# Kernel tuning notes

Hardware: AMD Instinct MI355X
Metric: run time of the kernel (lower is better)

## Reference

```python
import jax, jax.numpy as jnp
import numpy as np

N = 4096      # nodes
F = 32        # num_features (GATConv in = out per head)
H = 2         # heads
NHID = 64     # per-branch mlp output
C = 10        # num_classes
J = 3         # wavelet filters
E = 65536     # edges (avg degree 16)
G = 13        # num_gat = (3**3 - 1) // 2
NEG_SLOPE = 0.2


def setup_inputs() -> dict:
    key = jax.random.key(0)
    ks = jax.random.split(key, 12)
    sc = np.float32(1.0 / np.sqrt(N))
    g = np.float32(0.1)
    x = jax.random.normal(ks[0], (N, F), jnp.float32)
    edge_index = jax.random.randint(ks[1], (2, E), 0, N)
    U = jax.random.normal(ks[2], (N, N), jnp.float32) * sc
    psi = jax.random.normal(ks[3], (J, N, N), jnp.float32) * sc
    # 13 GATConv(F, F, heads=H) parameter stacks
    gat_W = jax.random.normal(ks[4], (G, F, H * F), jnp.float32) * g
    att_src = jax.random.normal(ks[5], (G, H, F), jnp.float32) * g
    att_dst = jax.random.normal(ks[6], (G, H, F), jnp.float32) * g
    gat_b = jnp.zeros((G, H * F), jnp.float32)
    # 13 branch MLPs: Linear(H*F -> NHID)
    mlp_W = jax.random.normal(ks[7], (G, H * F, NHID), jnp.float32) * g
    mlp_b = jnp.zeros((G, NHID), jnp.float32)
    # final head: Linear(13*NHID -> C)
    out_W = jax.random.normal(ks[8], (G * NHID, C), jnp.float32) * g
    out_b = jnp.zeros((C,), jnp.float32)
    return {"x": x, "edge_index": edge_index, "U": U, "psi": psi,
            "gat_W": gat_W, "att_src": att_src, "att_dst": att_dst,
            "gat_b": gat_b, "mlp_W": mlp_W, "mlp_b": mlp_b,
            "out_W": out_W, "out_b": out_b}


def _gat_branch(coef, W, a_s, a_d, bg, mw, mb, src, dst):
    # GATConv(F, F, heads=H, concat=True) in eval mode, then ELU + Linear.
    h = (coef @ W).reshape(N, H, F)                       # [N,H,F]
    es = jnp.einsum('nhf,hf->nh', h, a_s)                 # src attention logits
    ed = jnp.einsum('nhf,hf->nh', h, a_d)                 # dst attention logits
    e = jax.nn.leaky_relu(es[src] + ed[dst], NEG_SLOPE)   # [E+N,H]
    m = jax.ops.segment_max(e, dst, num_segments=N)       # stable softmax per dst
    w = jnp.exp(e - m[dst])
    z = jax.ops.segment_sum(w, dst, num_segments=N)
    alpha = w / (z[dst] + 1e-16)
    out = jax.ops.segment_sum(alpha[:, :, None] * h[src], dst, num_segments=N)
    out = out.reshape(N, H * F) + bg
    return jax.nn.elu(out) @ mw + mb                      # branch MLP -> [N,NHID]


def reference(x, edge_index, U, psi, gat_W, att_src, att_dst, gat_b,
              mlp_W, mlp_b, out_W, out_b):
    loops = jnp.arange(N)
    src = jnp.concatenate([edge_index[0], loops])         # add_self_loops
    dst = jnp.concatenate([edge_index[1], loops])
    # Scattering tree (layer=3, J=3): 1 + 3 + 9 = 13 coefficient maps.
    af = jnp.abs(x)
    coef0 = U @ af                                        # [N,F]
    y1 = jnp.einsum('jnm,mf->jnf', psi, af)               # level-1 wavelets [J,N,F]
    a1 = jnp.abs(y1)
    coef1 = jnp.einsum('nm,jmf->jnf', U, a1)              # [J,N,F]
    y2 = jnp.einsum('knm,jmf->jknf', psi, a1)             # level-2: psi_k @ |y1_j|
    coef2 = jnp.einsum('nm,jkmf->jknf', U, jnp.abs(y2)).reshape(J * J, N, F)
    coefs = jnp.concatenate([coef0[None], coef1, coef2], axis=0)  # [13,N,F]
    branch = jax.vmap(lambda c, W, a_s, a_d, bg, mw, mb:
                      _gat_branch(c, W, a_s, a_d, bg, mw, mb, src, dst))
    yb = branch(coefs, gat_W, att_src, att_dst, gat_b, mlp_W, mlp_b)  # [13,N,NHID]
    feat = jnp.moveaxis(yb, 0, 1).reshape(N, G * NHID)    # concat branches per node
    logits = jax.nn.elu(feat) @ out_W + out_b             # [N,C]
    return jax.nn.log_softmax(logits, axis=1)
```

## Files before the change

kernel.cpp:

```cpp
#include <hip/hip_runtime.h>
#include <hip/hip_bf16.h>

#define NN 4096
#define FF 32
#define EE 65536
#define GG 13

typedef float floatx4 __attribute__((ext_vector_type(4)));
typedef __bf16 bf16x8 __attribute__((ext_vector_type(8)));
typedef short short8 __attribute__((ext_vector_type(8)));

__device__ inline unsigned short f2bf(float f) {
    unsigned u = __float_as_uint(f);
    u += 0x7FFFu + ((u >> 16) & 1u);
    return (unsigned short)(u >> 16);
}


__global__ void k_prep1(const float* __restrict__ x, unsigned short* __restrict__ B) {
    int tid = blockIdx.x * 256 + threadIdx.x;
    int k = tid >> 5, col = tid & 31;
    float v = fabsf(x[tid]);
    B[(((k >> 5) * 2 + (col >> 4)) << 9) + ((col & 15) << 5) + (k & 31)] = f2bf(v);
}

__global__ void k_prep2(const float* __restrict__ P1, unsigned short* __restrict__ B) {
    int tid = blockIdx.x * 256 + threadIdx.x;
    int k = tid / 96, jf = tid % 96;
    int j = jf >> 5, f = jf & 31;
    float v = fabsf(P1[((1 + j) * NN + k) * FF + f]);
    B[(((k >> 5) * 6 + (jf >> 4)) << 9) + ((jf & 15) << 5) + (k & 31)] = f2bf(v);
}

__global__ void k_prep3(const float* __restrict__ P2, unsigned short* __restrict__ B) {
    int tid = blockIdx.x * 256 + threadIdx.x;
    int k = tid / 288, cc = tid % 288;
    int k3 = cc / 96, jf = cc % 96;
    float v = fabsf(P2[((1 + k3) * NN + k) * 96 + jf]);
    B[(((k >> 5) * 18 + (cc >> 4)) << 9) + ((cc & 15) << 5) + (k & 31)] = f2bf(v);
}

template <int NT>
__global__ __launch_bounds__(512) void k_pass(const float* __restrict__ Umat,
                                              const float* __restrict__ Psi,
                                              const unsigned short* __restrict__ Bfrag,
                                              float* __restrict__ Pout) {
    constexpr int NC = NT * 16;
    int tile = blockIdx.x;
    int mat = blockIdx.y;
    const float* A = (mat == 0) ? Umat : (Psi + (size_t)(mat - 1) * NN * NN);
    int tid = threadIdx.x;
    int wave = tid >> 6, lane = tid & 63;
    int c15 = lane & 15, q = lane >> 4;
    int row = tile * 16 + c15;
    const float* arow = A + (size_t)row * NN + wave * 512 + q * 8;
    const unsigned short* bbase = Bfrag + (size_t)(wave * 16) * NT * 512 + (c15 << 5) + (q << 3);

    floatx4 acc[NT];
#pragma unroll
    for (int t = 0; t < NT; t++) acc[t] = (floatx4){0.f, 0.f, 0.f, 0.f};

    floatx4 a0 = *(const floatx4*)arow;
    floatx4 a1 = *(const floatx4*)(arow + 4);

    for (int s = 0; s < 16; s++) {
        const unsigned short* bp = bbase + (size_t)s * NT * 512;
        short8 bv[NT];
#pragma unroll
        for (int t = 0; t < NT; t++) bv[t] = *(const short8*)(bp + t * 512);
        floatx4 n0 = {}, n1 = {};
        if (s < 15) {
            n0 = *(const floatx4*)(arow + (s + 1) * 32);
            n1 = *(const floatx4*)(arow + (s + 1) * 32 + 4);
        }
        short8 av;
        av[0] = f2bf(a0[0]); av[1] = f2bf(a0[1]); av[2] = f2bf(a0[2]); av[3] = f2bf(a0[3]);
        av[4] = f2bf(a1[0]); av[5] = f2bf(a1[1]); av[6] = f2bf(a1[2]); av[7] = f2bf(a1[3]);
        bf16x8 ab = __builtin_bit_cast(bf16x8, av);
#pragma unroll
        for (int t = 0; t < NT; t++)
            acc[t] = __builtin_amdgcn_mfma_f32_16x16x32_bf16(
                ab, __builtin_bit_cast(bf16x8, bv[t]), acc[t], 0, 0, 0);
        a0 = n0; a1 = n1;
    }

    __shared__ float cs[2][16 * NC];
    int half = wave & 1;
    for (int w2 = 0; w2 < 4; w2++) {
        if ((wave >> 1) == w2) {
#pragma unroll
            for (int t = 0; t < NT; t++)
#pragma unroll
                for (int r = 0; r < 4; r++) {
                    int idx = (q * 4 + r) * NC + t * 16 + c15;
                    if (w2 == 0) cs[half][idx] = acc[t][r];
                    else cs[half][idx] += acc[t][r];
                }
        }
        __syncthreads();
    }
    float* orow = Pout + ((size_t)mat * NN + (size_t)tile * 16) * NC;
    for (int i = tid; i < 16 * NC; i += 512) orow[i] = cs[0][i] + cs[1][i];
}

__global__ void k_hes(const float* __restrict__ P1, const float* __restrict__ P2,
                      const float* __restrict__ P3, const float* __restrict__ gatW,
                      const float* __restrict__ attS, const float* __restrict__ attD,
                      float* __restrict__ h, float* __restrict__ es,
                      float* __restrict__ ed) {
    int w = (blockIdx.x * 256 + threadIdx.x) >> 6;
    int lane = threadIdx.x & 63;
    int g = w >> 12, n = w & 4095;
    const float* crow;
    if (g == 0) crow = P1 + (size_t)n * FF;
    else if (g <= 3) crow = P2 + (size_t)n * 96 + (g - 1) * 32;
    else {
        int j = (g - 4) / 3, k3 = (g - 4) % 3;
        crow = P3 + (size_t)n * 288 + k3 * 96 + j * 32;
    }
    const float* wcol = gatW + g * (32 * 64) + lane;
    float a = 0.f;
#pragma unroll
    for (int f = 0; f < 32; f++) a += crow[f] * wcol[f * 64];
    h[(size_t)w * 64 + lane] = a;
    float vs = a * attS[g * 64 + lane];
    float vd = a * attD[g * 64 + lane];
#pragma unroll
    for (int off = 16; off >= 1; off >>= 1) {
        vs += __shfl_down(vs, off, 32);
        vd += __shfl_down(vd, off, 32);
    }
    if ((lane & 31) == 0) {
        es[w * 2 + (lane >> 5)] = vs;
        ed[w * 2 + (lane >> 5)] = vd;
    }
}

__global__ void k_hist(const int* __restrict__ ei, int* __restrict__ cnt) {
    int e = blockIdx.x * 256 + threadIdx.x;
    int d = (e < EE) ? ei[EE + e] : (e - EE);
    atomicAdd(&cnt[d], 1);
}

__global__ void k_scan(const int* __restrict__ cnt, int* __restrict__ offs,
                       int* __restrict__ cursor) {
    int lane = threadIdx.x;
    int base = lane * 64;
    int s = 0;
    for (int i = 0; i < 64; i++) s += cnt[base + i];
    int x = s;
    for (int d = 1; d < 64; d <<= 1) {
        int y = __shfl_up(x, d);
        if (lane >= d) x += y;
    }
    int run = x - s;
    for (int i = 0; i < 64; i++) {
        offs[base + i] = run;
        cursor[base + i] = run;
        run += cnt[base + i];
    }
}

__global__ void k_scatter(const int* __restrict__ ei, int* __restrict__ cursor,
                          int* __restrict__ csr) {
    int e = blockIdx.x * 256 + threadIdx.x;
    int s, d;
    if (e < EE) { s = ei[e]; d = ei[EE + e]; } else { s = d = e - EE; }
    int pos = atomicAdd(&cursor[d], 1);
    csr[pos] = s;
}

__global__ void k_gat(const float* __restrict__ h, const float* __restrict__ es,
                      const float* __restrict__ ed, const int* __restrict__ offs,
                      const int* __restrict__ cnt, const int* __restrict__ csr,
                      const float* __restrict__ gatb, float* __restrict__ gact) {
    int w = (blockIdx.x * 256 + threadIdx.x) >> 6;
    int lane = threadIdx.x & 63, hh = lane >> 5;
    int g = w >> 12, n = w & 4095;
    float myed = ed[w * 2 + hh];
    float bias = gatb[g * 64 + lane];
    int start = offs[n], deg = cnt[n];
    const float* hg = h + (size_t)g * NN * 64;
    const float* esg = es + (size_t)g * NN * 2;
    int sA = csr[start];
    int sB = (deg > 1) ? csr[start + 1] : 0;
    float hvA = hg[(size_t)sA * 64 + lane];
    float lgA = esg[sA * 2 + hh];
    float m = -INFINITY, z = 0.f, acc = 0.f;
    for (int i = 0; i < deg; i++) {
        int sC = (i + 2 < deg) ? csr[start + i + 2] : 0;
        float hvB = hg[(size_t)sB * 64 + lane];
        float lgB = esg[sB * 2 + hh];
        float lg = lgA + myed;
        lg = (lg > 0.f) ? lg : 0.2f * lg;
        float nm = fmaxf(m, lg);
        float sc = __expf(m - nm);
        float we = __expf(lg - nm);
        z = z * sc + we;
        acc = acc * sc + we * hvA;
        m = nm;
        sA = sB; sB = sC; hvA = hvB; lgA = lgB;
    }
    float o = acc / (z + 1e-16f) + bias;
    o = (o > 0.f) ? o : (__expf(o) - 1.f);
    gact[(size_t)w * 64 + lane] = o;
}

__global__ void k_mlp(const float* __restrict__ gact, const float* __restrict__ mlpW,
                      const float* __restrict__ mlpb, float* __restrict__ feat) {
    int tid = blockIdx.x * 256 + threadIdx.x;
    int g = tid >> 18;
    int n = (tid & ((1 << 18) - 1)) >> 6;
    int k = tid & 63;
    const float* grow = gact + ((size_t)g * NN + n) * 64;
    const float* wc = mlpW + (size_t)g * 64 * 64 + k;
    float a = mlpb[g * 64 + k];
#pragma unroll 8
    for (int i = 0; i < 64; i++) a += grow[i] * wc[i * 64];
    a = (a > 0.f) ? a : (__expf(a) - 1.f);
    feat[(size_t)n * 832 + g * 64 + k] = a;
}

__global__ void k_final(const float* __restrict__ feat, const float* __restrict__ oW,
                        const float* __restrict__ ob, float* __restrict__ out) {
    int w = (blockIdx.x * 256 + threadIdx.x) >> 6;
    int lane = threadIdx.x & 63;
    float a[10];
#pragma unroll
    for (int c = 0; c < 10; c++) a[c] = 0.f;
    const float* frow = feat + (size_t)w * 832;
#pragma unroll
    for (int i = 0; i < 13; i++) {
        float v = frow[i * 64 + lane];
        const float* wp = oW + (i * 64 + lane) * 10;
#pragma unroll
        for (int c = 0; c < 10; c++) a[c] += v * wp[c];
    }
#pragma unroll
    for (int off = 32; off >= 1; off >>= 1)
#pragma unroll
        for (int c = 0; c < 10; c++) a[c] += __shfl_down(a[c], off);
    if (lane == 0) {
        float m = -INFINITY;
#pragma unroll
        for (int c = 0; c < 10; c++) { a[c] += ob[c]; m = fmaxf(m, a[c]); }
        float s = 0.f;
#pragma unroll
        for (int c = 0; c < 10; c++) s += __expf(a[c] - m);
        float lse = m + __logf(s);
#pragma unroll
        for (int c = 0; c < 10; c++) out[w * 10 + c] = a[c] - lse;
    }
}

extern "C" void kernel_launch(void* const* d_in, const int* in_sizes, int n_in,
                              void* d_out, int out_size, void* d_ws, size_t ws_size,
                              hipStream_t stream) {
    const float* x    = (const float*)d_in[0];
    const int*   ei   = (const int*)d_in[1];
    const float* U    = (const float*)d_in[2];
    const float* psi  = (const float*)d_in[3];
    const float* gatW = (const float*)d_in[4];
    const float* attS = (const float*)d_in[5];
    const float* attD = (const float*)d_in[6];
    const float* gatb = (const float*)d_in[7];
    const float* mlpW = (const float*)d_in[8];
    const float* mlpb = (const float*)d_in[9];
    const float* oW   = (const float*)d_in[10];
    const float* ob   = (const float*)d_in[11];
    float* out = (float*)d_out;

    char* ws = (char*)d_ws;
    size_t off = 0;
    auto alloc = [&](size_t bytes) { char* p = ws + off; off += (bytes + 255) & ~(size_t)255; return p; };
    unsigned short* bf1 = (unsigned short*)alloc((size_t)NN * 32 * 2);
    float* P1           = (float*)alloc((size_t)4 * NN * 32 * 4);
    unsigned short* bf2 = (unsigned short*)alloc((size_t)NN * 96 * 2);
    float* P2           = (float*)alloc((size_t)4 * NN * 96 * 4);
    unsigned short* bf3 = (unsigned short*)alloc((size_t)NN * 288 * 2);
    float* P3           = (float*)alloc((size_t)NN * 288 * 4);
    float* h            = (float*)alloc((size_t)GG * NN * 64 * 4);
    float* es           = (float*)alloc((size_t)GG * NN * 2 * 4);
    float* ed           = (float*)alloc((size_t)GG * NN * 2 * 4);
    int* cnt            = (int*)alloc((size_t)NN * 4);
    int* offs           = (int*)alloc((size_t)NN * 4);
    int* cursor         = (int*)alloc((size_t)NN * 4);
    int* csr            = (int*)alloc((size_t)(EE + NN) * 4);
    float* gact         = (float*)alloc((size_t)GG * NN * 64 * 4);
    float* feat         = (float*)alloc((size_t)NN * 832 * 4);
    (void)ws_size; (void)in_sizes; (void)n_in; (void)out_size;

    hipMemsetAsync(cnt, 0, NN * 4, stream);
    k_hist<<<(EE + NN) / 256, 256, 0, stream>>>(ei, cnt);
    k_scan<<<1, 64, 0, stream>>>(cnt, offs, cursor);
    k_scatter<<<(EE + NN) / 256, 256, 0, stream>>>(ei, cursor, csr);

    k_prep1<<<(NN * 32) / 256, 256, 0, stream>>>(x, bf1);
    k_pass<2><<<dim3(NN / 16, 4), 512, 0, stream>>>(U, psi, bf1, P1);
    k_prep2<<<(NN * 96) / 256, 256, 0, stream>>>(P1, bf2);
    k_pass<6><<<dim3(NN / 16, 4), 512, 0, stream>>>(U, psi, bf2, P2);
    k_prep3<<<(NN * 288) / 256, 256, 0, stream>>>(P2, bf3);
    k_pass<18><<<dim3(NN / 16, 1), 512, 0, stream>>>(U, psi, bf3, P3);

    k_hes<<<(GG * NN * 64) / 256, 256, 0, stream>>>(P1, P2, P3, gatW, attS, attD, h, es, ed);
    k_gat<<<(GG * NN * 64) / 256, 256, 0, stream>>>(h, es, ed, offs, cnt, csr, gatb, gact);
    k_mlp<<<(GG * NN * 64) / 256, 256, 0, stream>>>(gact, mlpW, mlpb, feat);
    k_final<<<(NN * 64) / 256, 256, 0, stream>>>(feat, oW, ob, out);
}
```

Baseline: 670.2 us.

## Pack bf16 copies of U/psi in first pass and reuse in later passes

The first scattering pass writes its bf16-converted A fragments into a packed workspace buffer. The later passes read these packed bf16 fragments instead of re-reading and converting the fp32 matrices. The third pass is also split across column groups to raise block count and lower register use. This removes repeated fp32 reads and conversions, but it adds a large write in pass 1, needs a 128MB workspace, and re-reads U for each column group.

```diff
diff --git a/kernel.cpp b/kernel.cpp
--- a/kernel.cpp
+++ b/kernel.cpp
@@ -40,48 +40,120 @@
     B[(((k >> 5) * 18 + (cc >> 4)) << 9) + ((cc & 15) << 5) + (k & 31)] = f2bf(v);
 }
 
-template <int NT>
-__global__ __launch_bounds__(512) void k_pass(const float* __restrict__ Umat,
-                                              const float* __restrict__ Psi,
-                                              const unsigned short* __restrict__ Bfrag,
-                                              float* __restrict__ Pout) {
-    constexpr int NC = NT * 16;
+__global__ __launch_bounds__(512) void k_pass1(const float* __restrict__ Umat,
+                                               const float* __restrict__ Psi,
+                                               const unsigned short* __restrict__ Bfrag,
+                                               float* __restrict__ Pout,
+                                               unsigned short* __restrict__ Apack) {
     int tile = blockIdx.x;
     int mat = blockIdx.y;
     const float* A = (mat == 0) ? Umat : (Psi + (size_t)(mat - 1) * NN * NN);
     int tid = threadIdx.x;
     int wave = tid >> 6, lane = tid & 63;
     int c15 = lane & 15, q = lane >> 4;
-    int row = tile * 16 + c15;
-    const float* arow = A + (size_t)row * NN + wave * 512 + q * 8;
-    const unsigned short* bbase = Bfrag + (size_t)(wave * 16) * NT * 512 + (c15 << 5) + (q << 3);
-
-    floatx4 acc[NT];
-#pragma unroll
-    for (int t = 0; t < NT; t++) acc[t] = (floatx4){0.f, 0.f, 0.f, 0.f};
-
+    const float* arow = A + (size_t)(tile * 16 + c15) * NN + wave * 512 + q * 8;
+    const unsigned short* bbase = Bfrag + (size_t)(wave * 16) * 2 * 512 + (c15 << 5) + (q << 3);
+    unsigned short* apk = Apack + ((size_t)mat << 24) + (size_t)tile * 65536
+                          + (size_t)(wave * 16) * 512 + (c15 << 5) + (q << 3);
+
+    floatx4 acc0 = {0.f,0.f,0.f,0.f}, acc1 = {0.f,0.f,0.f,0.f};
     floatx4 a0 = *(const floatx4*)arow;
     floatx4 a1 = *(const floatx4*)(arow + 4);
-
-    for (int s = 0; s < 16; s++) {
-        const unsigned short* bp = bbase + (size_t)s * NT * 512;
-        short8 bv[NT];
-#pragma unroll
-        for (int t = 0; t < NT; t++) bv[t] = *(const short8*)(bp + t * 512);
-        floatx4 n0 = {}, n1 = {};
-        if (s < 15) {
-            n0 = *(const floatx4*)(arow + (s + 1) * 32);
-            n1 = *(const floatx4*)(arow + (s + 1) * 32 + 4);
-        }
+    short8 bv0 = *(const short8*)bbase;
+    short8 bv1 = *(const short8*)(bbase + 512);
+
+    for (int s = 0; s < 15; s++) {
+        floatx4 n0 = *(const floatx4*)(arow + (s + 1) * 32);
+        floatx4 n1 = *(const floatx4*)(arow + (s + 1) * 32 + 4);
+        const unsigned short* bp = bbase + (size_t)(s + 1) * 2 * 512;
+        short8 nb0 = *(const short8*)bp;
+        short8 nb1 = *(const short8*)(bp + 512);
         short8 av;
         av[0] = f2bf(a0[0]); av[1] = f2bf(a0[1]); av[2] = f2bf(a0[2]); av[3] = f2bf(a0[3]);
         av[4] = f2bf(a1[0]); av[5] = f2bf(a1[1]); av[6] = f2bf(a1[2]); av[7] = f2bf(a1[3]);
+        *(short8*)(apk + s * 512) = av;
         bf16x8 ab = __builtin_bit_cast(bf16x8, av);
+        acc0 = __builtin_amdgcn_mfma_f32_16x16x32_bf16(ab, __builtin_bit_cast(bf16x8, bv0), acc0, 0, 0, 0);
+        acc1 = __builtin_amdgcn_mfma_f32_16x16x32_bf16(ab, __builtin_bit_cast(bf16x8, bv1), acc1, 0, 0, 0);
+        a0 = n0; a1 = n1; bv0 = nb0; bv1 = nb1;
+    }
+    {
+        short8 av;
+        av[0] = f2bf(a0[0]); av[1] = f2bf(a0[1]); av[2] = f2bf(a0[2]); av[3] = f2bf(a0[3]);
+        av[4] = f2bf(a1[0]); av[5] = f2bf(a1[1]); av[6] = f2bf(a1[2]); av[7] = f2bf(a1[3]);
+        *(short8*)(apk + 15 * 512) = av;
+        bf16x8 ab = __builtin_bit_cast(bf16x8, av);
+        acc0 = __builtin_amdgcn_mfma_f32_16x16x32_bf16(ab, __builtin_bit_cast(bf16x8, bv0), acc0, 0, 0, 0);
+        acc1 = __builtin_amdgcn_mfma_f32_16x16x32_bf16(ab, __builtin_bit_cast(bf16x8, bv1), acc1, 0, 0, 0);
+    }
+
+    __shared__ float cs[2][16 * 32];
+    int half = wave & 1;
+    floatx4 acc[2] = {acc0, acc1};
+    for (int w2 = 0; w2 < 4; w2++) {
+        if ((wave >> 1) == w2) {
+#pragma unroll
+            for (int t = 0; t < 2; t++)
+#pragma unroll
+                for (int r = 0; r < 4; r++) {
+                    int idx = (q * 4 + r) * 32 + t * 16 + c15;
+                    if (w2 == 0) cs[half][idx] = acc[t][r];
+                    else cs[half][idx] += acc[t][r];
+                }
+        }
+        __syncthreads();
+    }
+    float* orow = Pout + ((size_t)mat * NN + (size_t)tile * 16) * 32;
+    for (int i = tid; i < 16 * 32; i += 512) orow[i] = cs[0][i] + cs[1][i];
+}
+
+template <int NT, int NTOT>
+__global__ __launch_bounds__(512) void k_passP(const unsigned short* __restrict__ Apack,
+                                               const unsigned short* __restrict__ Bfrag,
+                                               float* __restrict__ Pout) {
+    constexpr int NC = NT * 16;
+    constexpr int NCTOT = NTOT * 16;
+    int tile = blockIdx.x;
+    int mat = blockIdx.y;
+    int cg = blockIdx.z;
+    int tid = threadIdx.x;
+    int wave = tid >> 6, lane = tid & 63;
+    int c15 = lane & 15, q = lane >> 4;
+    const unsigned short* ap = Apack + ((size_t)mat << 24) + (size_t)tile * 65536
+                               + (size_t)(wave * 16) * 512 + (c15 << 5) + (q << 3);
+    const unsigned short* bbase = Bfrag + (size_t)(wave * 16) * NTOT * 512
+                                  + (size_t)(cg * NT) * 512 + (c15 << 5) + (q << 3);
+
+    floatx4 acc[NT];
+#pragma unroll
+    for (int t = 0; t < NT; t++) acc[t] = (floatx4){0.f, 0.f, 0.f, 0.f};
+
+    short8 af = *(const short8*)ap;
+    short8 bv[NT];
+#pragma unroll
+    for (int t = 0; t < NT; t++) bv[t] = *(const short8*)(bbase + t * 512);
+
+    for (int s = 0; s < 15; s++) {
+        short8 af2 = *(const short8*)(ap + (s + 1) * 512);
+        short8 bv2[NT];
+        const unsigned short* bp = bbase + (size_t)(s + 1) * NTOT * 512;
+#pragma unroll
+        for (int t = 0; t < NT; t++) bv2[t] = *(const short8*)(bp + t * 512);
+        bf16x8 ab = __builtin_bit_cast(bf16x8, af);
 #pragma unroll
         for (int t = 0; t < NT; t++)
             acc[t] = __builtin_amdgcn_mfma_f32_16x16x32_bf16(
                 ab, __builtin_bit_cast(bf16x8, bv[t]), acc[t], 0, 0, 0);
-        a0 = n0; a1 = n1;
+        af = af2;
+#pragma unroll
+        for (int t = 0; t < NT; t++) bv[t] = bv2[t];
+    }
+    {
+        bf16x8 ab = __builtin_bit_cast(bf16x8, af);
+#pragma unroll
+        for (int t = 0; t < NT; t++)
+            acc[t] = __builtin_amdgcn_mfma_f32_16x16x32_bf16(
+                ab, __builtin_bit_cast(bf16x8, bv[t]), acc[t], 0, 0, 0);
     }
 
     __shared__ float cs[2][16 * NC];
@@ -99,8 +171,11 @@
         }
         __syncthreads();
     }
-    float* orow = Pout + ((size_t)mat * NN + (size_t)tile * 16) * NC;
-    for (int i = tid; i < 16 * NC; i += 512) orow[i] = cs[0][i] + cs[1][i];
+    float* orow = Pout + ((size_t)mat * NN + (size_t)tile * 16) * NCTOT + cg * NC;
+    for (int i = tid; i < 16 * NC; i += 512) {
+        int r = i / NC, c = i % NC;
+        orow[(size_t)r * NCTOT + c] = cs[0][i] + cs[1][i];
+    }
 }
 
 __global__ void k_hes(const float* __restrict__ P1, const float* __restrict__ P2,
@@ -273,6 +348,7 @@
     char* ws = (char*)d_ws;
     size_t off = 0;
     auto alloc = [&](size_t bytes) { char* p = ws + off; off += (bytes + 255) & ~(size_t)255; return p; };
+    unsigned short* Apack = (unsigned short*)alloc((size_t)4 * NN * NN * 2);
     unsigned short* bf1 = (unsigned short*)alloc((size_t)NN * 32 * 2);
     float* P1           = (float*)alloc((size_t)4 * NN * 32 * 4);
     unsigned short* bf2 = (unsigned short*)alloc((size_t)NN * 96 * 2);
@@ -296,11 +372,11 @@
     k_scatter<<<(EE + NN) / 256, 256, 0, stream>>>(ei, cursor, csr);
 
     k_prep1<<<(NN * 32) / 256, 256, 0, stream>>>(x, bf1);
-    k_pass<2><<<dim3(NN / 16, 4), 512, 0, stream>>>(U, psi, bf1, P1);
+    k_pass1<<<dim3(NN / 16, 4), 512, 0, stream>>>(U, psi, bf1, P1, Apack);
     k_prep2<<<(NN * 96) / 256, 256, 0, stream>>>(P1, bf2);
-    k_pass<6><<<dim3(NN / 16, 4), 512, 0, stream>>>(U, psi, bf2, P2);
+    k_passP<6, 6><<<dim3(NN / 16, 4, 1), 512, 0, stream>>>(Apack, bf2, P2);
     k_prep3<<<(NN * 288) / 256, 256, 0, stream>>>(P2, bf3);
-    k_pass<18><<<dim3(NN / 16, 1), 512, 0, stream>>>(U, psi, bf3, P3);
+    k_passP<6, 18><<<dim3(NN / 16, 1, 3), 512, 0, stream>>>(Apack, bf3, P3);
 
     k_hes<<<(GG * NN * 64) / 256, 256, 0, stream>>>(P1, P2, P3, gatW, attS, attD, h, es, ed);
     k_gat<<<(GG * NN * 64) / 256, 256, 0, stream>>>(h, es, ed, offs, cnt, csr, gatb, gact);
```

Result: faster. 656.4 us (-2.1%).
